# Performance work log

Hardware: AMD Instinct MI355X
Metric: run time of the kernel (lower is better)

## Reference

```python
import jax, jax.numpy as jnp
import numpy as np

DT = 0.05      # bsde.delta_t
EPS = 1e-6     # BatchNormalization epsilon


def _bn(x, gamma, beta):
    # training-mode batch norm: statistics over the batch axis
    m = jnp.mean(x, axis=0, keepdims=True)
    v = jnp.var(x, axis=0, keepdims=True)
    return (x - m) * jax.lax.rsqrt(v + EPS) * gamma + beta


def _subnet(x, g0, b0, W0, g1, b1, W1, g2, b2, W2, bias2, g3, b3):
    # bn -> (dense -> bn -> relu) x 2 -> dense(+bias) -> bn
    x = _bn(x, g0, b0)
    x = jax.nn.relu(_bn(x @ W0, g1, b1))
    x = jax.nn.relu(_bn(x @ W1, g2, b2))
    x = _bn(x @ W2 + bias2, g3, b3)
    return x


def setup_inputs() -> dict:
    key = jax.random.key(0)
    B, D, N, H = 8192, 100, 20, 110
    T = N - 1  # number of subnets
    ks = jax.random.split(key, 18)
    u = lambda k, s, lo, hi: jax.random.uniform(k, s, jnp.float32, lo, hi)
    s_dh = np.sqrt(2.0 / (D + H)).astype(np.float32)
    s_hh = np.sqrt(2.0 / (H + H)).astype(np.float32)
    s_hd = np.sqrt(2.0 / (H + D)).astype(np.float32)
    return {
        "dw": jax.random.normal(ks[0], (B, D, N), jnp.float32) * np.sqrt(DT).astype(np.float32),
        "x": jax.random.normal(ks[1], (B, D, N + 1), jnp.float32),
        "mean_y_input": jax.random.normal(ks[2], (N,), jnp.float32),
        "y_init": u(ks[3], (1,), 0.0, 1.0),
        "z_init": u(ks[4], (1, D), -0.1, 0.1),
        "gamma0": u(ks[5], (T, D), 0.1, 0.5),
        "beta0": 0.1 * jax.random.normal(ks[6], (T, D), jnp.float32),
        "W0": s_dh * jax.random.normal(ks[7], (T, D, H), jnp.float32),
        "gamma1": u(ks[8], (T, H), 0.1, 0.5),
        "beta1": 0.1 * jax.random.normal(ks[9], (T, H), jnp.float32),
        "W1": s_hh * jax.random.normal(ks[10], (T, H, H), jnp.float32),
        "gamma2": u(ks[11], (T, H), 0.1, 0.5),
        "beta2": 0.1 * jax.random.normal(ks[12], (T, H), jnp.float32),
        "W2": s_hd * jax.random.normal(ks[13], (T, H, D), jnp.float32),
        "bias2": jnp.zeros((T, D), jnp.float32),
        "gamma3": u(ks[14], (T, D), 0.1, 0.5),
        "beta3": 0.1 * jax.random.normal(ks[15], (T, D), jnp.float32),
    }


def reference(dw, x, mean_y_input, y_init, z_init, gamma0, beta0, W0,
              gamma1, beta1, W1, gamma2, beta2, W2, bias2, gamma3, beta3):
    B, D, N = dw.shape
    T = N - 1
    # z at step t+1 depends only on x[:, :, t+1] and subnet t -> compute all in parallel
    x_steps = jnp.moveaxis(x[:, :, 1:N], 2, 0)  # [T, B, D]
    z_all = jax.vmap(_subnet)(x_steps, gamma0, beta0, W0, gamma1, beta1, W1,
                              gamma2, beta2, W2, bias2, gamma3, beta3) / D  # [T, B, D]
    z0 = jnp.broadcast_to(z_init, (B, D))          # all_one_vec @ z_init
    zs = jnp.concatenate([z0[None], z_all], axis=0)  # [N, B, D] (z used at each update)
    dw_steps = jnp.moveaxis(dw, 2, 0)               # [N, B, D]
    y0 = jnp.ones((B, 1), dw.dtype) * y_init

    def step(y, zd):
        z, dwt = zd
        # f_tf(t, x, y, z) = sin(y) for the SineBM equation
        y_new = y - DT * jnp.sin(y) + jnp.sum(z * dwt, axis=1, keepdims=True)
        return y_new, jnp.mean(y_new)

    y_final, means = jax.lax.scan(step, y0, (zs, dw_steps))
    mean_y = jnp.concatenate([jnp.mean(y0)[None], means[:T]])  # length N
    return y_final, mean_y
```

## Files before the change

kernel.cpp:

```cpp
#include <hip/hip_runtime.h>

typedef unsigned short u16;
typedef unsigned int   u32;

#define BATCH  8192
#define DIM    100
#define HID    110
#define TSUB   19
#define NSTEP  20
#define KP     128
#define NPAD   112
#define BN_EPS 1e-6f
#define DT_C   0.05f

#define SAB  1024
#define SAR  8
#define SLICES 32
#define NBLK_SCAN 2048
#define NMT  64

typedef __bf16 v8bf __attribute__((ext_vector_type(8)));
typedef float  v4f  __attribute__((ext_vector_type(4)));
typedef float  v2f  __attribute__((ext_vector_type(2)));
typedef u16    u16x4 __attribute__((ext_vector_type(4)));

__device__ __forceinline__ u16 f2bf(float f) {
    u32 u = __float_as_uint(f);
    return (u16)((u + 0x7fffu + ((u >> 16) & 1u)) >> 16);
}
__device__ __forceinline__ float bf2f(u16 h) {
    return __uint_as_float(((u32)h) << 16);
}

__global__ __launch_bounds__(256, 4)
void statsA(const float* __restrict__ x, float* __restrict__ part,
            u32* __restrict__ xT32) {
    __shared__ u16 xls[4][2112];
    const int tid = threadIdx.x;
    const int b0 = blockIdx.x * SAR;
    const int tt = (tid < 13) ? tid : 12;

    float s[8], q[8];
#pragma unroll
    for (int j = 0; j < 8; j++) { s[j] = 0.f; q[j] = 0.f; }
    float4 s2 = {0,0,0,0}, q2 = {0,0,0,0};

#pragma unroll
    for (int g = 0; g < 2; g++) {
        v4f va[4], vb[4], vc[4];
#pragma unroll
        for (int r = 0; r < 4; r++) {
            const float* base  = x + (size_t)(b0 + g * 4 + r) * 2100;
            const float* amain = base + 8 * tid;
            const float* atail = base + 2048 + 4 * tt;
            asm volatile("global_load_dwordx4 %0, %1, off"           : "=v"(va[r]) : "v"(amain));
            asm volatile("global_load_dwordx4 %0, %1, off offset:16" : "=v"(vb[r]) : "v"(amain));
            asm volatile("global_load_dwordx4 %0, %1, off"           : "=v"(vc[r]) : "v"(atail));
        }
        asm volatile("s_waitcnt vmcnt(0)" ::: "memory");
        __builtin_amdgcn_sched_barrier(0);
#pragma unroll
        for (int r = 0; r < 4; r++) {
#pragma unroll
            for (int j = 0; j < 4; j++) {
                float a = va[r][j], b = vb[r][j];
                s[j]     += a; q[j]     += a * a;
                s[4 + j] += b; q[4 + j] += b * b;
            }
            u16 pk[8];
#pragma unroll
            for (int j = 0; j < 4; j++) { pk[j] = f2bf(va[r][j]); pk[4 + j] = f2bf(vb[r][j]); }
            *(uint4*)&xls[r][tid * 8] = *(uint4*)pk;
            if (tid < 13) {
                float4 c = { vc[r][0], vc[r][1], vc[r][2], vc[r][3] };
                s2.x += c.x; s2.y += c.y; s2.z += c.z; s2.w += c.w;
                q2.x += c.x * c.x; q2.y += c.y * c.y; q2.z += c.z * c.z; q2.w += c.w * c.w;
                u16x4 p2 = { f2bf(c.x), f2bf(c.y), f2bf(c.z), f2bf(c.w) };
                *(u16x4*)&xls[r][2048 + tid * 4] = p2;
            }
        }
        __syncthreads();
        const int TOT4 = TSUB * 4 * (NPAD / 2);
        for (int i = tid; i < TOT4; i += 256) {
            int w = i % (NPAD / 2);
            int seg = i / (NPAD / 2);
            int r = seg & 3, t = seg >> 2;
            int d0 = w * 2;
            u32 v = 0;
            if (d0 < DIM) {
                u16 lo = xls[r][d0 * 21 + t + 1];
                u16 hi = (d0 + 1 < DIM) ? xls[r][(d0 + 1) * 21 + t + 1] : (u16)0;
                v = (u32)lo | ((u32)hi << 16);
            }
            xT32[((size_t)t * BATCH + b0 + g * 4 + r) * (NPAD / 2) + w] = v;
        }
        __syncthreads();
    }

    float* ps = part + (size_t)blockIdx.x * 4200;
    *(float4*)&ps[8 * tid]            = *(float4*)&s[0];
    *(float4*)&ps[8 * tid + 4]        = *(float4*)&s[4];
    *(float4*)&ps[2100 + 8 * tid]     = *(float4*)&q[0];
    *(float4*)&ps[2100 + 8 * tid + 4] = *(float4*)&q[4];
    if (tid < 13) {
        *(float4*)&ps[2048 + 4 * tid] = s2;
        *(float4*)&ps[4148 + 4 * tid] = q2;
    }
}

__global__ void statsB(const float* __restrict__ part, float* __restrict__ slpart) {
    int gid = blockIdx.x * 256 + threadIdx.x;
    if (gid >= 4200 * SLICES) return;
    int slice = gid / 4200;
    int o = gid - slice * 4200;
    const float* p = part + (size_t)slice * (SAB / SLICES) * 4200 + o;
    float acc = 0.f;
#pragma unroll 8
    for (int i = 0; i < SAB / SLICES; i++) acc += p[(size_t)i * 4200];
    slpart[(size_t)slice * 4200 + o] = acc;
}

__global__ void wtrans(const float* __restrict__ W0, const float* __restrict__ W1,
                       const float* __restrict__ W2, u16* __restrict__ WTsw) {
    __shared__ float lw[HID * HID];
    const int t = blockIdx.x, l = blockIdx.y, tid = threadIdx.x;
    const float* W; int K, N;
    if (l == 0)      { W = W0; K = DIM; N = HID; }
    else if (l == 1) { W = W1; K = HID; N = HID; }
    else             { W = W2; K = HID; N = DIM; }
    const float* Wt = W + (size_t)t * K * N;
    for (int i = tid; i < K * N; i += 256) lw[i] = Wt[i];
    __syncthreads();
    u16* out = WTsw + ((size_t)l * TSUB + t) * (NPAD * KP);
    for (int i = tid; i < NPAD * 16; i += 256) {
        int n = i / 16, p = i % 16;
        int kc = p ^ (n & 7);
        u16 o8[8];
#pragma unroll
        for (int j = 0; j < 8; j++) {
            int k = kc * 8 + j;
            float v = (k < K && n < N) ? lw[k * N + n] : 0.f;
            o8[j] = f2bf(v);
        }
        *(uint4*)&out[(size_t)n * KP + p * 8] = *(uint4*)o8;
    }
}

__global__ void finalize0(const float* __restrict__ slpart, const float* __restrict__ g0,
                          float* __restrict__ aff0) {
    const int t = blockIdx.x, tid = threadIdx.x;
    float a = 0.f;
    if (tid < DIM) {
        int idx = tid * 21 + (t + 1);
        float s = 0.f, q = 0.f;
#pragma unroll 8
        for (int s2 = 0; s2 < SLICES; s2++) {
            s += slpart[(size_t)s2 * 4200 + idx];
            q += slpart[(size_t)s2 * 4200 + 2100 + idx];
        }
        float m = s * (1.f / BATCH);
        float v = q * (1.f / BATCH) - m * m;
        a = g0[t * DIM + tid] * rsqrtf(v + BN_EPS);
    }
    aff0[(size_t)t * 2 * KP + tid]      = a;
    aff0[(size_t)t * 2 * KP + KP + tid] = 0.f;
}

template <int KREAL>
__global__ void finalizeAff(const float* __restrict__ partIn,
                            const float* __restrict__ g, const float* __restrict__ b,
                            float* __restrict__ aff) {
    const int t = blockIdx.x, tid = threadIdx.x;
    float a = 0.f, c = 0.f;
    if (tid < KREAL) {
        float s = 0.f, q = 0.f;
#pragma unroll 8
        for (int m2 = 0; m2 < NMT; m2++) {
            const float* pp = partIn + ((size_t)(m2 * TSUB + t) * 2) * NPAD;
            s += pp[tid];
            q += pp[NPAD + tid];
        }
        float m = s * (1.f / BATCH);
        float v = q * (1.f / BATCH) - m * m;
        float rstd = rsqrtf(v + BN_EPS);
        float ga = g[t * KREAL + tid] * rstd;
        a = ga;
        c = b[t * KREAL + tid] - m * ga;
    }
    aff[(size_t)t * 2 * KP + tid]      = a;
    aff[(size_t)t * 2 * KP + KP + tid] = c;
}

template <int RELU, int BMAJOR>
__global__ __launch_bounds__(512, 4)
void gemm_kernel(const u16* __restrict__ Ain,
                 const u16* __restrict__ WTswL,
                 const float* __restrict__ aff,
                 u16* __restrict__ Hout,
                 float* __restrict__ partOut) {
    __shared__ __align__(16) u16 Blds[NPAD * KP];
    __shared__ float s_sum[NPAD], s_sq[NPAD];
    __shared__ float aAffL[KP], cAffL[KP];

    const int tid = threadIdx.x;
    const int mt = blockIdx.x;
    const int t  = blockIdx.y;
    const int brow0 = mt * 128;

    if (tid < NPAD) { s_sum[tid] = 0.f; s_sq[tid] = 0.f; }
    if (tid < KP) {
        aAffL[tid] = aff[(size_t)t * 2 * KP + tid];
        cAffL[tid] = aff[(size_t)t * 2 * KP + KP + tid];
    }

    {
        const uint4* wsrc = (const uint4*)(WTswL + (size_t)t * NPAD * KP);
        uint4* bl = (uint4*)Blds;
        for (int i = tid; i < NPAD * KP / 8; i += 512) bl[i] = wsrc[i];
    }
    __syncthreads();

    const int lane = tid & 63;
    const int wv   = tid >> 6;
    const int r0   = lane & 15;
    const int q    = lane >> 4;
    const int row  = wv * 16 + r0;

    const u16* arow = Ain + ((size_t)t * BATCH + brow0 + row) * NPAD;
    u16 hv[4][8];
#pragma unroll
    for (int ks = 0; ks < 4; ks++) {
        int cb = ks * 4 + q;
        int cbl = (cb > 13) ? 13 : cb;
        *(uint4*)hv[ks] = *(const uint4*)(arow + cbl * 8);
    }
    v8bf afr[4];
#pragma unroll
    for (int ks = 0; ks < 4; ks++) {
        int cb = ks * 4 + q;
        const float* ap = &aAffL[cb * 8];
        const float* cp = &cAffL[cb * 8];
        u16 pk[8];
#pragma unroll
        for (int j = 0; j < 8; j++) {
            float av = fmaf(bf2f(hv[ks][j]), ap[j], cp[j]);
            if (RELU) av = fmaxf(av, 0.f);
            pk[j] = f2bf(av);
        }
        afr[ks] = *(v8bf*)pk;
    }

    v4f acc[7];
#pragma unroll
    for (int j = 0; j < 7; j++) { v4f z = {0.f, 0.f, 0.f, 0.f}; acc[j] = z; }
#pragma unroll
    for (int ks = 0; ks < 4; ks++) {
        int cbase = ks * 4 + q;
#pragma unroll
        for (int nf = 0; nf < 7; nf++) {
            int nr = nf * 16 + r0;
            v8bf bfr = *(const v8bf*)&Blds[nr * KP + ((cbase ^ (nr & 7)) * 8)];
            acc[nf] = __builtin_amdgcn_mfma_f32_16x16x32_bf16(afr[ks], bfr, acc[nf], 0, 0, 0);
        }
    }

#pragma unroll
    for (int nf = 0; nf < 7; nf++) {
        int n = nf * 16 + r0;
#pragma unroll
        for (int rg = 0; rg < 4; rg++) {
            int grow = brow0 + wv * 16 + q * 4 + rg;
            size_t oidx = BMAJOR ? ((size_t)grow * (TSUB * NPAD) + (size_t)t * NPAD + n)
                                 : (((size_t)t * BATCH + grow) * NPAD + n);
            Hout[oidx] = f2bf(acc[nf][rg]);
        }
    }
#pragma unroll
    for (int nf = 0; nf < 7; nf++) {
        float cs = 0.f, cq = 0.f;
#pragma unroll
        for (int rg = 0; rg < 4; rg++) {
            float vv = acc[nf][rg];
            cs += vv; cq += vv * vv;
        }
        cs += __shfl_xor(cs, 16); cs += __shfl_xor(cs, 32);
        cq += __shfl_xor(cq, 16); cq += __shfl_xor(cq, 32);
        if (q == 0) {
            atomicAdd(&s_sum[nf * 16 + r0], cs);
            atomicAdd(&s_sq[nf * 16 + r0], cq);
        }
    }
    __syncthreads();
    if (tid < NPAD) {
        float* pp = partOut + ((size_t)(mt * TSUB + t) * 2) * NPAD;
        pp[tid]        = s_sum[tid];
        pp[NPAD + tid] = s_sq[tid];
    }
}

__global__ void finalize3(const float* __restrict__ partIn,
                          const float* __restrict__ g3, const float* __restrict__ b3,
                          float4* __restrict__ acg) {
    int i = blockIdx.x * 256 + threadIdx.x;
    if (i >= TSUB * 50) return;
    int t = i / 50, p = i - t * 50;
    float4 o;
#pragma unroll
    for (int h = 0; h < 2; h++) {
        int d = 2 * p + h;
        float s = 0.f, q = 0.f;
#pragma unroll 8
        for (int m2 = 0; m2 < NMT; m2++) {
            const float* pp = partIn + ((size_t)(m2 * TSUB + t) * 2) * NPAD;
            s += pp[d];
            q += pp[NPAD + d];
        }
        float m = s * (1.f / BATCH);
        float v = q * (1.f / BATCH) - m * m;
        float rstd = rsqrtf(v + BN_EPS);
        int e = t * DIM + d;
        float ga = g3[e] * rstd * (1.f / DIM);
        float cc = b3[e] * (1.f / DIM) - m * ga;
        if (h == 0) { o.x = ga; o.y = cc; } else { o.z = ga; o.w = cc; }
    }
    acg[i] = o;
}

__global__ __launch_bounds__(256, 4)
void scan_kernel(const float* __restrict__ dw,
                 const u16* __restrict__ zbuf,
                 const float4* __restrict__ acg,
                 const float* __restrict__ z_init, const float* __restrict__ y_init,
                 float* __restrict__ yout, float* __restrict__ mred) {
    __shared__ float bsum[NSTEP];
    const int tid = threadIdx.x;
    if (tid < NSTEP) bsum[tid] = 0.f;
    __syncthreads();

    const int wv = tid >> 6, lane = tid & 63;
    const int b = blockIdx.x * 4 + wv;
    const int ll = (lane < 50) ? lane : 49;

    v4f w[10];
    u32 zr[TSUB];
    v2f zi;
    {
        const float* dwaddr = dw + (size_t)b * (DIM * NSTEP) + ll * 40;
        const u16*   zaddr  = zbuf + (size_t)b * (TSUB * NPAD) + 2 * ll;
        const float* ziaddr = z_init + 2 * ll;
        asm volatile("global_load_dwordx4 %0, %1, off offset:0"   : "=v"(w[0]) : "v"(dwaddr));
        asm volatile("global_load_dwordx4 %0, %1, off offset:16"  : "=v"(w[1]) : "v"(dwaddr));
        asm volatile("global_load_dwordx4 %0, %1, off offset:32"  : "=v"(w[2]) : "v"(dwaddr));
        asm volatile("global_load_dwordx4 %0, %1, off offset:48"  : "=v"(w[3]) : "v"(dwaddr));
        asm volatile("global_load_dwordx4 %0, %1, off offset:64"  : "=v"(w[4]) : "v"(dwaddr));
        asm volatile("global_load_dwordx4 %0, %1, off offset:80"  : "=v"(w[5]) : "v"(dwaddr));
        asm volatile("global_load_dwordx4 %0, %1, off offset:96"  : "=v"(w[6]) : "v"(dwaddr));
        asm volatile("global_load_dwordx4 %0, %1, off offset:112" : "=v"(w[7]) : "v"(dwaddr));
        asm volatile("global_load_dwordx4 %0, %1, off offset:128" : "=v"(w[8]) : "v"(dwaddr));
        asm volatile("global_load_dwordx4 %0, %1, off offset:144" : "=v"(w[9]) : "v"(dwaddr));
#pragma unroll
        for (int t = 0; t < TSUB; t++)
            asm volatile("global_load_dword %0, %1, off offset:%2"
                         : "=v"(zr[t]) : "v"(zaddr), "i"(t * NPAD * 2));
        asm volatile("global_load_dwordx2 %0, %1, off" : "=v"(zi) : "v"(ziaddr));
        asm volatile("s_waitcnt vmcnt(0)" ::: "memory");
        __builtin_amdgcn_sched_barrier(0);
    }

    float acc[NSTEP];
#pragma unroll
    for (int k = 0; k < NSTEP; k++) acc[k] = 0.f;
    if (lane < 50) {
        acc[0] = zi[0] * w[0][0] + zi[1] * w[5][0];
#pragma unroll
        for (int t = 0; t < TSUB; t++) {
            float4 ac = acg[t * 50 + ll];
            u32 z = zr[t];
            float za0 = fmaf(bf2f((u16)(z & 0xffffu)), ac.x, ac.y);
            float za1 = fmaf(bf2f((u16)(z >> 16)),     ac.z, ac.w);
            const int n = t + 1, j = n >> 2, k = n & 3;
            acc[n] += w[j][k] * za0 + w[5 + j][k] * za1;
        }
    }

#pragma unroll
    for (int m = 1; m < 64; m <<= 1) {
#pragma unroll
        for (int k = 0; k < NSTEP; k++) acc[k] += __shfl_xor(acc[k], m, 64);
    }

    const float yi = y_init[0];
    float y = yi, ysave = 0.f;
#pragma unroll
    for (int i = 0; i < NSTEP; i++) {
        y = y - DT_C * __sinf(y) + acc[i];
        if (i == lane - 1) ysave = y;
    }
    if (lane == 0) yout[b] = y;
    if (lane >= 1 && lane < NSTEP) atomicAdd(&bsum[lane], ysave);
    __syncthreads();
    if (tid >= 1 && tid < NSTEP) mred[blockIdx.x * NSTEP + tid] = bsum[tid];
}

__global__ void meanred(const float* __restrict__ mred, const float* __restrict__ y_init,
                        float* __restrict__ meanout) {
    const int n = blockIdx.x, tid = threadIdx.x;
    if (n == 0) { if (tid == 0) meanout[0] = y_init[0]; return; }
    float s = 0.f;
    for (int i = tid; i < NBLK_SCAN; i += 256) s += mred[(size_t)i * NSTEP + n];
#pragma unroll
    for (int m = 1; m < 64; m <<= 1) s += __shfl_xor(s, m, 64);
    __shared__ float ws4[4];
    if ((tid & 63) == 0) ws4[tid >> 6] = s;
    __syncthreads();
    if (tid == 0) meanout[n] = (ws4[0] + ws4[1] + ws4[2] + ws4[3]) * (1.f / BATCH);
}

extern "C" void kernel_launch(void* const* d_in, const int* in_sizes, int n_in,
                              void* d_out, int out_size, void* d_ws, size_t ws_size,
                              hipStream_t stream) {
    const float* dw     = (const float*)d_in[0];
    const float* x      = (const float*)d_in[1];
    const float* y_init = (const float*)d_in[3];
    const float* z_init = (const float*)d_in[4];
    const float* g0 = (const float*)d_in[5];
    const float* W0 = (const float*)d_in[7];
    const float* g1 = (const float*)d_in[8];
    const float* b1 = (const float*)d_in[9];
    const float* W1 = (const float*)d_in[10];
    const float* g2 = (const float*)d_in[11];
    const float* b2 = (const float*)d_in[12];
    const float* W2 = (const float*)d_in[13];
    const float* g3 = (const float*)d_in[15];
    const float* b3 = (const float*)d_in[16];

    char* ws = (char*)d_ws;
    size_t off = 0;
    auto alloc = [&](size_t bytes) -> void* {
        off = (off + 255) & ~(size_t)255;
        void* p = ws + off;
        off += bytes;
        return p;
    };

    float* slpart = (float*)alloc((size_t)SLICES * 4200 * 4);
    float* gp0    = (float*)alloc((size_t)NMT * TSUB * 2 * NPAD * 4);
    float* gp1    = (float*)alloc((size_t)NMT * TSUB * 2 * NPAD * 4);
    float* aff0   = (float*)alloc((size_t)TSUB * 2 * KP * 4);
    float* aff1   = (float*)alloc((size_t)TSUB * 2 * KP * 4);
    float* aff2   = (float*)alloc((size_t)TSUB * 2 * KP * 4);

    u16* WTsw = (u16*)alloc((size_t)3 * TSUB * NPAD * KP * 2);
    float4* acg = (float4*)alloc((size_t)TSUB * 50 * 16);
    float* mred = (float*)alloc((size_t)NBLK_SCAN * NSTEP * 4);

    const size_t hBytes = (size_t)TSUB * BATCH * NPAD * 2;
    u16* h0 = (u16*)alloc(hBytes);
    u16* h1 = (u16*)alloc(hBytes);
    u16* outbuf = h0;
    float* part = (float*)h0;
    u32*  xT32  = (u32*)h1;

    float* yout = (float*)d_out;
    float* meanout = yout + BATCH;

    wtrans<<<dim3(TSUB, 3), 256, 0, stream>>>(W0, W1, W2, WTsw);
    statsA<<<SAB, 256, 0, stream>>>(x, part, xT32);
    statsB<<<(4200 * SLICES + 255) / 256, 256, 0, stream>>>(part, slpart);
    finalize0<<<TSUB, 128, 0, stream>>>(slpart, g0, aff0);

    const u16* xT = (const u16*)xT32;
    u16* WT0 = WTsw;
    u16* WT1 = WTsw + (size_t)TSUB * NPAD * KP;
    u16* WT2 = WTsw + (size_t)2 * TSUB * NPAD * KP;

    gemm_kernel<0, 0><<<dim3(NMT, TSUB), 512, 0, stream>>>(xT, WT0, aff0, h0, gp0);
    finalizeAff<HID><<<TSUB, 128, 0, stream>>>(gp0, g1, b1, aff1);
    gemm_kernel<1, 0><<<dim3(NMT, TSUB), 512, 0, stream>>>(h0, WT1, aff1, h1, gp1);
    finalizeAff<HID><<<TSUB, 128, 0, stream>>>(gp1, g2, b2, aff2);
    gemm_kernel<1, 1><<<dim3(NMT, TSUB), 512, 0, stream>>>(h1, WT2, aff2, outbuf, gp0);

    finalize3<<<4, 256, 0, stream>>>(gp0, g3, b3, acg);
    scan_kernel<<<NBLK_SCAN, 256, 0, stream>>>(dw, outbuf, acg, z_init, y_init, yout, mred);
    meanred<<<NSTEP, 256, 0, stream>>>(mred, y_init, meanout);
}
```

Before: 170.6 us.

## Coalesce dw loads and replace shuffle reduction with LDS-staged dot products

Each lane now loads dw in a strided pattern: consecutive lanes read consecutive 16-byte chunks, and each lane covers 4 time steps at 10 dimensions. The affine-transformed z values are staged in shared memory so every lane can compute partial dots for its time steps. Partial sums go to LDS and are reduced per step, replacing the 20x6 cross-lane shuffle butterfly. This trades shuffle ALU work and scattered loads for extra LDS traffic. It relies on wave-level lgkmcnt waits rather than barriers, which is valid only because each wave touches just its own LDS slice.

```diff
diff --git a/kernel.cpp b/kernel.cpp
--- a/kernel.cpp
+++ b/kernel.cpp
@@ -18,6 +18,8 @@
 #define SLICES 32
 #define NBLK_SCAN 2048
 #define NMT  64
+
+#define ZSTR 106
 
 typedef __bf16 v8bf __attribute__((ext_vector_type(8)));
 typedef float  v4f  __attribute__((ext_vector_type(4)));
@@ -332,6 +334,9 @@
                  const float4* __restrict__ acg,
                  const float* __restrict__ z_init, const float* __restrict__ y_init,
                  float* __restrict__ yout, float* __restrict__ mred) {
+    __shared__ float zsh[4][20][ZSTR];
+    __shared__ float psum[4][NSTEP][10];
+    __shared__ float dotv[4][NSTEP];
     __shared__ float bsum[NSTEP];
     const int tid = threadIdx.x;
     if (tid < NSTEP) bsum[tid] = 0.f;
@@ -340,24 +345,27 @@
     const int wv = tid >> 6, lane = tid & 63;
     const int b = blockIdx.x * 4 + wv;
     const int ll = (lane < 50) ? lane : 49;
+    const int nq = ll % 5;
+    const int dg = ll / 5;
 
     v4f w[10];
     u32 zr[TSUB];
     v2f zi;
     {
-        const float* dwaddr = dw + (size_t)b * (DIM * NSTEP) + ll * 40;
+        const float* a1 = dw + (size_t)b * (DIM * NSTEP) + ll * 4;
+        const float* a2 = a1 + 1000;
         const u16*   zaddr  = zbuf + (size_t)b * (TSUB * NPAD) + 2 * ll;
         const float* ziaddr = z_init + 2 * ll;
-        asm volatile("global_load_dwordx4 %0, %1, off offset:0"   : "=v"(w[0]) : "v"(dwaddr));
-        asm volatile("global_load_dwordx4 %0, %1, off offset:16"  : "=v"(w[1]) : "v"(dwaddr));
-        asm volatile("global_load_dwordx4 %0, %1, off offset:32"  : "=v"(w[2]) : "v"(dwaddr));
-        asm volatile("global_load_dwordx4 %0, %1, off offset:48"  : "=v"(w[3]) : "v"(dwaddr));
-        asm volatile("global_load_dwordx4 %0, %1, off offset:64"  : "=v"(w[4]) : "v"(dwaddr));
-        asm volatile("global_load_dwordx4 %0, %1, off offset:80"  : "=v"(w[5]) : "v"(dwaddr));
-        asm volatile("global_load_dwordx4 %0, %1, off offset:96"  : "=v"(w[6]) : "v"(dwaddr));
-        asm volatile("global_load_dwordx4 %0, %1, off offset:112" : "=v"(w[7]) : "v"(dwaddr));
-        asm volatile("global_load_dwordx4 %0, %1, off offset:128" : "=v"(w[8]) : "v"(dwaddr));
-        asm volatile("global_load_dwordx4 %0, %1, off offset:144" : "=v"(w[9]) : "v"(dwaddr));
+        asm volatile("global_load_dwordx4 %0, %1, off offset:0"    : "=v"(w[0]) : "v"(a1));
+        asm volatile("global_load_dwordx4 %0, %1, off offset:800"  : "=v"(w[1]) : "v"(a1));
+        asm volatile("global_load_dwordx4 %0, %1, off offset:1600" : "=v"(w[2]) : "v"(a1));
+        asm volatile("global_load_dwordx4 %0, %1, off offset:2400" : "=v"(w[3]) : "v"(a1));
+        asm volatile("global_load_dwordx4 %0, %1, off offset:3200" : "=v"(w[4]) : "v"(a1));
+        asm volatile("global_load_dwordx4 %0, %1, off offset:0"    : "=v"(w[5]) : "v"(a2));
+        asm volatile("global_load_dwordx4 %0, %1, off offset:800"  : "=v"(w[6]) : "v"(a2));
+        asm volatile("global_load_dwordx4 %0, %1, off offset:1600" : "=v"(w[7]) : "v"(a2));
+        asm volatile("global_load_dwordx4 %0, %1, off offset:2400" : "=v"(w[8]) : "v"(a2));
+        asm volatile("global_load_dwordx4 %0, %1, off offset:3200" : "=v"(w[9]) : "v"(a2));
 #pragma unroll
         for (int t = 0; t < TSUB; t++)
             asm volatile("global_load_dword %0, %1, off offset:%2"
@@ -367,33 +375,58 @@
         __builtin_amdgcn_sched_barrier(0);
     }
 
-    float acc[NSTEP];
-#pragma unroll
-    for (int k = 0; k < NSTEP; k++) acc[k] = 0.f;
     if (lane < 50) {
-        acc[0] = zi[0] * w[0][0] + zi[1] * w[5][0];
 #pragma unroll
         for (int t = 0; t < TSUB; t++) {
             float4 ac = acg[t * 50 + ll];
-            u32 z = zr[t];
-            float za0 = fmaf(bf2f((u16)(z & 0xffffu)), ac.x, ac.y);
-            float za1 = fmaf(bf2f((u16)(z >> 16)),     ac.z, ac.w);
-            const int n = t + 1, j = n >> 2, k = n & 3;
-            acc[n] += w[j][k] * za0 + w[5 + j][k] * za1;
-        }
-    }
-
-#pragma unroll
-    for (int m = 1; m < 64; m <<= 1) {
-#pragma unroll
-        for (int k = 0; k < NSTEP; k++) acc[k] += __shfl_xor(acc[k], m, 64);
-    }
+            zsh[wv][t][2 * ll]     = fmaf(bf2f((u16)(zr[t] & 0xffffu)), ac.x, ac.y);
+            zsh[wv][t][2 * ll + 1] = fmaf(bf2f((u16)(zr[t] >> 16)),     ac.z, ac.w);
+        }
+        zsh[wv][19][2 * ll]     = zi[0];
+        zsh[wv][19][2 * ll + 1] = zi[1];
+    }
+    asm volatile("s_waitcnt lgkmcnt(0)" ::: "memory");
+    __builtin_amdgcn_sched_barrier(0);
+
+    float acc4[4] = {0.f, 0.f, 0.f, 0.f};
+    if (lane < 50) {
+        int rows[4];
+#pragma unroll
+        for (int k = 0; k < 4; k++) {
+            int n = 4 * nq + k;
+            rows[k] = (n == 0) ? 19 : (n - 1);
+        }
+#pragma unroll
+        for (int j = 0; j < 10; j++) {
+            int d = dg + 10 * j;
+#pragma unroll
+            for (int k = 0; k < 4; k++)
+                acc4[k] += w[j][k] * zsh[wv][rows[k]][d];
+        }
+#pragma unroll
+        for (int k = 0; k < 4; k++) psum[wv][4 * nq + k][dg] = acc4[k];
+    }
+    asm volatile("s_waitcnt lgkmcnt(0)" ::: "memory");
+    __builtin_amdgcn_sched_barrier(0);
+
+    if (lane < NSTEP) {
+        float sdot = 0.f;
+#pragma unroll
+        for (int g2 = 0; g2 < 10; g2++) sdot += psum[wv][lane][g2];
+        dotv[wv][lane] = sdot;
+    }
+    asm volatile("s_waitcnt lgkmcnt(0)" ::: "memory");
+    __builtin_amdgcn_sched_barrier(0);
+
+    float dots[NSTEP];
+#pragma unroll
+    for (int i = 0; i < NSTEP; i++) dots[i] = dotv[wv][i];
 
     const float yi = y_init[0];
     float y = yi, ysave = 0.f;
 #pragma unroll
     for (int i = 0; i < NSTEP; i++) {
-        y = y - DT_C * __sinf(y) + acc[i];
+        y = y - DT_C * __sinf(y) + dots[i];
         if (i == lane - 1) ysave = y;
     }
     if (lane == 0) yout[b] = y;
```

Result: no change. 172.8 us (+1.3%).
